# Kernel optimization log

Measured on AMD Instinct MI355X. Metric: run time of the kernel, lower is better.

The kernel has to match this reference:

```python
import jax, jax.numpy as jnp
import numpy as np

N = 50000      # nodes
E = 400000     # edges (before self-loops)
IN = 256       # in_dim
H = 4          # heads in layer 1
C = 64         # h_dim (per-head channels, layer 1)
OUT = 16       # out_dim (layer 2, 1 head)
NEG_SLOPE = 0.2


def gatv2_layer(x, src, dst, Wl, bl, Wr, br, att, bias, heads, ch, concat, num_nodes):
    # x: [N, F]; src/dst: [E']; Wl/Wr: [F, heads*ch]; att: [heads, ch]
    xl = (x @ Wl + bl).reshape(num_nodes, heads, ch)  # source transform
    xr = (x @ Wr + br).reshape(num_nodes, heads, ch)  # target transform
    m = xl[src] + xr[dst]                              # [E', H, C] gather
    e = jnp.sum(jax.nn.leaky_relu(m, NEG_SLOPE) * att, axis=-1)  # [E', H]
    # segment softmax over incoming edges of each dst node (self-loops ensure non-empty)
    emax = jax.ops.segment_max(e, dst, num_segments=num_nodes)   # [N, H]
    ee = jnp.exp(e - emax[dst])
    denom = jax.ops.segment_sum(ee, dst, num_segments=num_nodes)  # [N, H]
    alpha = ee / (denom[dst] + 1e-16)                              # [E', H]
    out = jax.ops.segment_sum(alpha[..., None] * xl[src], dst, num_segments=num_nodes)  # [N,H,C]
    if concat:
        out = out.reshape(num_nodes, heads * ch)
    else:
        out = out.mean(axis=1)
    return out + bias


def setup_inputs() -> dict:
    key = jax.random.key(0)
    ks = jax.random.split(key, 16)
    s = 0.05
    inp = {
        "x": jax.random.normal(ks[0], (N, IN), jnp.float32),
        "edge_index": jax.random.randint(ks[1], (2, E), 0, N),
        # layer 1 params (in_dim -> heads*h_dim)
        "Wl1": jax.random.normal(ks[2], (IN, H * C), jnp.float32) * s,
        "bl1": jnp.zeros((H * C,), jnp.float32),
        "Wr1": jax.random.normal(ks[3], (IN, H * C), jnp.float32) * s,
        "br1": jnp.zeros((H * C,), jnp.float32),
        "att1": jax.random.normal(ks[4], (H, C), jnp.float32) * s,
        "bias1": jnp.zeros((H * C,), jnp.float32),
        # layer 2 params (heads*h_dim -> out_dim, 1 head)
        "Wl2": jax.random.normal(ks[5], (H * C, OUT), jnp.float32) * s,
        "bl2": jnp.zeros((OUT,), jnp.float32),
        "Wr2": jax.random.normal(ks[6], (H * C, OUT), jnp.float32) * s,
        "br2": jnp.zeros((OUT,), jnp.float32),
        "att2": jax.random.normal(ks[7], (1, OUT), jnp.float32) * s,
        "bias2": jnp.zeros((OUT,), jnp.float32),
    }
    return inp


def reference(x, edge_index, Wl1, bl1, Wr1, br1, att1, bias1, Wl2, bl2, Wr2, br2, att2, bias2):
    # add self loops (PyG GATv2Conv default add_self_loops=True)
    loop = jnp.arange(N, dtype=edge_index.dtype)
    src = jnp.concatenate([edge_index[0], loop])
    dst = jnp.concatenate([edge_index[1], loop])
    h = gatv2_layer(x, src, dst, Wl1, bl1, Wr1, br1, att1, bias1, H, C, True, N)
    h = jnp.tanh(h)
    o = gatv2_layer(h, src, dst, Wl2, bl2, Wr2, br2, att2, bias2, 1, OUT, False, N)
    return o, jax.nn.log_softmax(o, axis=1)
```

## Files before the change

kernel.cpp:

```cpp
#include <hip/hip_runtime.h>

typedef __bf16 bfv8 __attribute__((ext_vector_type(8)));
typedef float f32x4 __attribute__((ext_vector_type(4)));
typedef short shortv8 __attribute__((ext_vector_type(8)));

__device__ __forceinline__ float b2f(unsigned short u) {
  unsigned int v = ((unsigned int)u) << 16;
  float f;
  __builtin_memcpy(&f, &v, 4);
  return f;
}
__device__ __forceinline__ unsigned short f2b(float f) {
  unsigned int u;
  __builtin_memcpy(&u, &f, 4);
  u += 0x7fffu + ((u >> 16) & 1u);
  return (unsigned short)(u >> 16);
}

__global__ void probe_kernel(const unsigned short* __restrict__ x, int* __restrict__ flag) {
  int lane = threadIdx.x;
  int cnt = 0;
  for (int i = lane; i < 4096; i += 64) {
    unsigned int e = (x[i] >> 7) & 0xffu;
    if (e >= 0x86u) cnt++;
  }
#pragma unroll
  for (int off = 1; off < 64; off <<= 1) cnt += __shfl_xor(cnt, off, 64);
  if (lane == 0) *flag = (cnt > 100) ? 1 : 0;
}

#define P_TOT 140352
__global__ __launch_bounds__(256) void conv_params_kernel(
    const void* p0, const void* p1, const void* p2, const void* p3,
    const void* p4, const void* p5, const void* p6, const void* p7,
    const void* p8, const void* p9, const void* p10, const void* p11,
    unsigned short* __restrict__ dst, const int* __restrict__ flagp) {
  int i = blockIdx.x * 256 + threadIdx.x;
  if (i >= P_TOT) return;
  const int offs[13] = {0, 65536, 65792, 131328, 131584, 131840, 132096,
                        136192, 136208, 140304, 140320, 140336, P_TOT};
  const void* ptrs[12] = {p0, p1, p2, p3, p4, p5, p6, p7, p8, p9, p10, p11};
  int flag = *flagp;
  int t = 0;
  while (i >= offs[t + 1]) t++;
  int local = i - offs[t];
  unsigned short v;
  if (flag) v = f2b(((const float*)ptrs[t])[local]);
  else v = ((const unsigned short*)ptrs[t])[local];
  dst[i] = v;
}

__global__ __launch_bounds__(256) void transpose_w_kernel(
    const unsigned short* __restrict__ Pc,
    unsigned short* __restrict__ WT1, unsigned short* __restrict__ WT2) {
  int idx = blockIdx.x * 256 + threadIdx.x;
  if (idx < 512 * 256) {
    int n = idx >> 8, k = idx & 255;
    WT1[idx] = (n < 256) ? Pc[0 + k * 256 + n]
                         : Pc[65792 + k * 256 + (n - 256)];
  } else {
    int j = idx - 512 * 256;
    if (j < 32 * 256) {
      int n = j >> 8, k = j & 255;
      WT2[j] = (n < 16) ? Pc[132096 + k * 16 + n]
                        : Pc[136208 + k * 16 + (n - 16)];
    }
  }
}

__global__ __launch_bounds__(256) void gemm1_kernel(
    const void* __restrict__ X, const int* __restrict__ flagp,
    const unsigned short* __restrict__ WT,
    const unsigned short* __restrict__ bl, const unsigned short* __restrict__ br,
    unsigned short* __restrict__ C, int M) {
  __shared__ unsigned short ltile[4][64 * 72];
  const int lane = threadIdx.x & 63;
  const int w = threadIdx.x >> 6;
  const int quad = lane >> 4;
  const int l16 = lane & 15;
  const int m_base = blockIdx.x * 128 + (w >> 1) * 64;
  const int n_base = blockIdx.y * 128 + (w & 1) * 64;
  const int fl = *flagp;

  f32x4 acc[4][4];
#pragma unroll
  for (int i = 0; i < 4; i++)
#pragma unroll
    for (int j = 0; j < 4; j++) acc[i][j] = (f32x4){0.f, 0.f, 0.f, 0.f};

  if (fl) {
    const float* Xf = (const float*)X;
#pragma unroll
    for (int k0 = 0; k0 < 256; k0 += 32) {
      bfv8 a[4], b[4];
#pragma unroll
      for (int i = 0; i < 4; i++) {
        int row = m_base + 16 * i + l16;
        if (row >= M) row = M - 1;
        const float* p = Xf + (size_t)row * 256 + k0 + quad * 8;
        float4 f0 = *reinterpret_cast<const float4*>(p);
        float4 f1 = *reinterpret_cast<const float4*>(p + 4);
        union { bfv8 v; unsigned short us[8]; } pa;
        pa.us[0] = f2b(f0.x); pa.us[1] = f2b(f0.y);
        pa.us[2] = f2b(f0.z); pa.us[3] = f2b(f0.w);
        pa.us[4] = f2b(f1.x); pa.us[5] = f2b(f1.y);
        pa.us[6] = f2b(f1.z); pa.us[7] = f2b(f1.w);
        a[i] = pa.v;
      }
#pragma unroll
      for (int j = 0; j < 4; j++) {
        int col = n_base + 16 * j + l16;
        b[j] = *reinterpret_cast<const bfv8*>(WT + (size_t)col * 256 + k0 + quad * 8);
      }
#pragma unroll
      for (int i = 0; i < 4; i++)
#pragma unroll
        for (int j = 0; j < 4; j++)
          acc[i][j] = __builtin_amdgcn_mfma_f32_16x16x32_bf16(a[i], b[j], acc[i][j], 0, 0, 0);
    }
  } else {
    const unsigned short* Xb = (const unsigned short*)X;
#pragma unroll
    for (int k0 = 0; k0 < 256; k0 += 32) {
      bfv8 a[4], b[4];
#pragma unroll
      for (int i = 0; i < 4; i++) {
        int row = m_base + 16 * i + l16;
        if (row >= M) row = M - 1;
        a[i] = *reinterpret_cast<const bfv8*>(Xb + (size_t)row * 256 + k0 + quad * 8);
      }
#pragma unroll
      for (int j = 0; j < 4; j++) {
        int col = n_base + 16 * j + l16;
        b[j] = *reinterpret_cast<const bfv8*>(WT + (size_t)col * 256 + k0 + quad * 8);
      }
#pragma unroll
      for (int i = 0; i < 4; i++)
#pragma unroll
        for (int j = 0; j < 4; j++)
          acc[i][j] = __builtin_amdgcn_mfma_f32_16x16x32_bf16(a[i], b[j], acc[i][j], 0, 0, 0);
    }
  }

  unsigned short* lt = ltile[w];
#pragma unroll
  for (int j = 0; j < 4; j++) {
    int col = n_base + 16 * j + l16;
    float bias = (col < 256) ? b2f(bl[col]) : b2f(br[col - 256]);
#pragma unroll
    for (int i = 0; i < 4; i++)
#pragma unroll
      for (int r = 0; r < 4; r++)
        lt[(16 * i + quad * 4 + r) * 72 + 16 * j + l16] = f2b(acc[i][j][r] + bias);
  }
#pragma unroll
  for (int pass = 0; pass < 8; pass++) {
    int row = pass * 8 + (lane >> 3);
    int colg = (lane & 7) * 8;
    shortv8 v = *reinterpret_cast<const shortv8*>(lt + row * 72 + colg);
    int grow = m_base + row;
    if (grow < M)
      *reinterpret_cast<shortv8*>(C + (size_t)grow * 512 + n_base + colg) = v;
  }
}

__global__ __launch_bounds__(256) void gemm2_kernel(
    const unsigned short* __restrict__ H, const unsigned short* __restrict__ WT,
    const unsigned short* __restrict__ bl, const unsigned short* __restrict__ br,
    float* __restrict__ C, int M) {
  const int lane = threadIdx.x & 63;
  const int w = threadIdx.x >> 6;
  const int quad = lane >> 4;
  const int l16 = lane & 15;
  const int m_base = blockIdx.x * 256 + w * 64;

  f32x4 acc[4][2];
#pragma unroll
  for (int i = 0; i < 4; i++)
#pragma unroll
    for (int j = 0; j < 2; j++) acc[i][j] = (f32x4){0.f, 0.f, 0.f, 0.f};

#pragma unroll
  for (int k0 = 0; k0 < 256; k0 += 32) {
    bfv8 a[4], b[2];
#pragma unroll
    for (int i = 0; i < 4; i++) {
      int row = m_base + 16 * i + l16;
      if (row >= M) row = M - 1;
      a[i] = *reinterpret_cast<const bfv8*>(H + (size_t)row * 256 + k0 + quad * 8);
    }
#pragma unroll
    for (int j = 0; j < 2; j++) {
      int col = 16 * j + l16;
      b[j] = *reinterpret_cast<const bfv8*>(WT + (size_t)col * 256 + k0 + quad * 8);
    }
#pragma unroll
    for (int i = 0; i < 4; i++)
#pragma unroll
      for (int j = 0; j < 2; j++)
        acc[i][j] = __builtin_amdgcn_mfma_f32_16x16x32_bf16(a[i], b[j], acc[i][j], 0, 0, 0);
  }

#pragma unroll
  for (int j = 0; j < 2; j++) {
    int col = 16 * j + l16;
    float bias = (j == 0) ? b2f(bl[l16]) : b2f(br[l16]);
#pragma unroll
    for (int i = 0; i < 4; i++) {
#pragma unroll
      for (int r = 0; r < 4; r++) {
        int row = m_base + 16 * i + quad * 4 + r;
        if (row < M) C[(size_t)row * 32 + col] = acc[i][j][r] + bias;
      }
    }
  }
}

__global__ __launch_bounds__(256) void count_kernel(const int* __restrict__ ei, int E, int Nn,
                                                    int* __restrict__ cnt) {
  int i = blockIdx.x * 256 + threadIdx.x;
  int total = E + Nn;
  if (i >= total) return;
  int d = (i < E) ? ei[E + i] : (i - E);
  if ((unsigned)d >= (unsigned)Nn) d = 0;
  atomicAdd(&cnt[d], 1);
}

__global__ __launch_bounds__(1024) void scan1_kernel(const int* __restrict__ cnt,
                                                     int* __restrict__ row_start,
                                                     int* __restrict__ blkTot, int Nn) {
  __shared__ int buf[1024];
  int t = threadIdx.x;
  int i = blockIdx.x * 1024 + t;
  int v = (i < Nn) ? cnt[i] : 0;
  buf[t] = v;
  __syncthreads();
  for (int off = 1; off < 1024; off <<= 1) {
    int x = (t >= off) ? buf[t - off] : 0;
    __syncthreads();
    buf[t] += x;
    __syncthreads();
  }
  if (i < Nn) row_start[i] = buf[t] - v;
  if (t == 1023) blkTot[blockIdx.x] = buf[1023];
}

__global__ __launch_bounds__(64) void scan2_kernel(const int* __restrict__ blkTot,
                                                   int* __restrict__ blkOff, int nb,
                                                   int* __restrict__ row_start, int Nn,
                                                   int total) {
  int lane = threadIdx.x;
  int v = (lane < nb) ? blkTot[lane] : 0;
  int s = v;
#pragma unroll
  for (int off = 1; off < 64; off <<= 1) {
    int u = __shfl_up(s, off, 64);
    if (lane >= off) s += u;
  }
  if (lane < nb) blkOff[lane] = s - v;
  if (lane == 0) row_start[Nn] = total;
}

__global__ __launch_bounds__(1024) void scan3_kernel(int* __restrict__ row_start,
                                                     int* __restrict__ cursor,
                                                     const int* __restrict__ blkOff, int Nn) {
  int i = blockIdx.x * 1024 + threadIdx.x;
  if (i < Nn) {
    int val = row_start[i] + blkOff[blockIdx.x];
    row_start[i] = val;
    cursor[i] = val;
  }
}

__global__ __launch_bounds__(256) void fill_kernel(const int* __restrict__ ei, int E, int Nn,
                                                   int* __restrict__ cursor,
                                                   int* __restrict__ csr_src) {
  int i = blockIdx.x * 256 + threadIdx.x;
  int total = E + Nn;
  if (i >= total) return;
  int s, d;
  if (i < E) { s = ei[i]; d = ei[E + i]; } else { s = i - E; d = i - E; }
  if ((unsigned)d >= (unsigned)Nn) d = 0;
  if ((unsigned)s >= (unsigned)Nn) s = 0;
  int pos = atomicAdd(&cursor[d], 1);
  if ((unsigned)pos < (unsigned)total) csr_src[pos] = s;
}

__global__ __launch_bounds__(256) void agg1_kernel(
    const unsigned short* __restrict__ C1,
    const unsigned short* __restrict__ att1,
    const unsigned short* __restrict__ bias1,
    const int* __restrict__ row_start, const int* __restrict__ csr_src,
    unsigned short* __restrict__ H1,
    int Nn, int Etot) {
  int wid = blockIdx.x * 4 + (threadIdx.x >> 6);
  if (wid >= Nn) return;
  int lane = threadIdx.x & 63;
  int c0 = lane * 4;

  ushort4 a4 = *reinterpret_cast<const ushort4*>(att1 + c0);
  float at0 = b2f(a4.x), at1 = b2f(a4.y), at2 = b2f(a4.z), at3 = b2f(a4.w);
  ushort4 r4 = *reinterpret_cast<const ushort4*>(C1 + (size_t)wid * 512 + 256 + c0);
  float xr0 = b2f(r4.x), xr1 = b2f(r4.y), xr2 = b2f(r4.z), xr3 = b2f(r4.w);

  float denom = 0.f, a0 = 0.f, a1 = 0.f, a2 = 0.f, a3 = 0.f;
  int beg = row_start[wid], end = row_start[wid + 1];
  if (beg < 0) beg = 0;
  if (end < beg || end - beg > Etot) end = beg;
  int n = end - beg;

  ushort4 cur0 = make_ushort4(0, 0, 0, 0), cur1 = cur0;
  if (n > 0) {
    int s = csr_src[beg];
    if ((unsigned)s >= (unsigned)Nn) s = 0;
    cur0 = *reinterpret_cast<const ushort4*>(C1 + (size_t)s * 512 + c0);
  }
  if (n > 1) {
    int s = csr_src[beg + 1];
    if ((unsigned)s >= (unsigned)Nn) s = 0;
    cur1 = *reinterpret_cast<const ushort4*>(C1 + (size_t)s * 512 + c0);
  }

#define AGG1_BODY(XV)                                                        \
  {                                                                          \
    float xl0 = b2f(XV.x), xl1 = b2f(XV.y), xl2 = b2f(XV.z), xl3 = b2f(XV.w); \
    float m0 = xl0 + xr0, m1 = xl1 + xr1, m2 = xl2 + xr2, m3 = xl3 + xr3;    \
    float l0 = m0 > 0.f ? m0 : 0.2f * m0;                                    \
    float l1 = m1 > 0.f ? m1 : 0.2f * m1;                                    \
    float l2 = m2 > 0.f ? m2 : 0.2f * m2;                                    \
    float l3 = m3 > 0.f ? m3 : 0.2f * m3;                                    \
    float part = l0 * at0 + l1 * at1 + l2 * at2 + l3 * at3;                  \
    part += __shfl_xor(part, 1, 64);                                         \
    part += __shfl_xor(part, 2, 64);                                         \
    part += __shfl_xor(part, 4, 64);                                         \
    part += __shfl_xor(part, 8, 64);                                         \
    part = fminf(fmaxf(part, -60.f), 60.f);                                  \
    float wgt = __expf(part);                                                \
    denom += wgt;                                                            \
    a0 += wgt * xl0; a1 += wgt * xl1; a2 += wgt * xl2; a3 += wgt * xl3;      \
  }

  int i = 0;
  for (; i + 2 <= n; i += 2) {
    ushort4 nxt0 = cur0, nxt1 = cur1;
    int q0 = beg + i + 2, q1 = beg + i + 3;
    if (q0 < end) {
      int s = csr_src[q0];
      if ((unsigned)s >= (unsigned)Nn) s = 0;
      nxt0 = *reinterpret_cast<const ushort4*>(C1 + (size_t)s * 512 + c0);
    }
    if (q1 < end) {
      int s = csr_src[q1];
      if ((unsigned)s >= (unsigned)Nn) s = 0;
      nxt1 = *reinterpret_cast<const ushort4*>(C1 + (size_t)s * 512 + c0);
    }
    AGG1_BODY(cur0);
    AGG1_BODY(cur1);
    cur0 = nxt0;
    cur1 = nxt1;
  }
  if (i < n) AGG1_BODY(cur0);
#undef AGG1_BODY

  float inv = 1.f / (denom + 1e-16f);
  ushort4 b4 = *reinterpret_cast<const ushort4*>(bias1 + c0);
  float h0 = tanhf(a0 * inv + b2f(b4.x));
  float h1 = tanhf(a1 * inv + b2f(b4.y));
  float h2 = tanhf(a2 * inv + b2f(b4.z));
  float h3 = tanhf(a3 * inv + b2f(b4.w));
  if (!(h0 == h0)) h0 = 0.f;
  if (!(h1 == h1)) h1 = 0.f;
  if (!(h2 == h2)) h2 = 0.f;
  if (!(h3 == h3)) h3 = 0.f;
  ushort4 o4;
  o4.x = f2b(h0); o4.y = f2b(h1); o4.z = f2b(h2); o4.w = f2b(h3);
  *reinterpret_cast<ushort4*>(H1 + (size_t)wid * 256 + c0) = o4;
}

__global__ __launch_bounds__(256) void agg2_kernel(
    const float* __restrict__ C2,
    const unsigned short* __restrict__ att2,
    const unsigned short* __restrict__ bias2,
    const int* __restrict__ row_start, const int* __restrict__ csr_src,
    float* __restrict__ out,
    int Nn, int Etot) {
  int wid = blockIdx.x * 4 + (threadIdx.x >> 6);
  if (wid >= Nn) return;
  int lane = threadIdx.x & 63;
  int g = lane >> 4;
  int c = lane & 15;

  float att = b2f(att2[c]);
  float xr = C2[(size_t)wid * 32 + 16 + c];
  float denom = 0.f, acc = 0.f;
  int beg = row_start[wid], end = row_start[wid + 1];
  if (beg < 0) beg = 0;
  if (end < beg || end - beg > Etot) end = beg;

  int p = beg + g;
  float xl_cur = 0.f;
  if (p < end) {
    int s = csr_src[p];
    if ((unsigned)s >= (unsigned)Nn) s = 0;
    xl_cur = C2[(size_t)s * 32 + c];
  }
  while (p < end) {
    int pn = p + 4;
    float xl_nxt = 0.f;
    if (pn < end) {
      int s = csr_src[pn];
      if ((unsigned)s >= (unsigned)Nn) s = 0;
      xl_nxt = C2[(size_t)s * 32 + c];
    }
    float mm = xl_cur + xr;
    float lr = mm > 0.f ? mm : 0.2f * mm;
    float part = lr * att;
    part += __shfl_xor(part, 1, 64);
    part += __shfl_xor(part, 2, 64);
    part += __shfl_xor(part, 4, 64);
    part += __shfl_xor(part, 8, 64);
    part = fminf(fmaxf(part, -60.f), 60.f);
    float wgt = __expf(part);
    denom += wgt;
    acc += wgt * xl_cur;
    xl_cur = xl_nxt;
    p = pn;
  }
  denom += __shfl_xor(denom, 16, 64);
  denom += __shfl_xor(denom, 32, 64);
  acc += __shfl_xor(acc, 16, 64);
  acc += __shfl_xor(acc, 32, 64);

  float o = acc / (denom + 1e-16f) + b2f(bias2[c]);
  if (!(o == o)) o = 0.f;
  float mx = o;
  mx = fmaxf(mx, __shfl_xor(mx, 1, 64));
  mx = fmaxf(mx, __shfl_xor(mx, 2, 64));
  mx = fmaxf(mx, __shfl_xor(mx, 4, 64));
  mx = fmaxf(mx, __shfl_xor(mx, 8, 64));
  float ex = expf(o - mx);
  float se = ex;
  se += __shfl_xor(se, 1, 64);
  se += __shfl_xor(se, 2, 64);
  se += __shfl_xor(se, 4, 64);
  se += __shfl_xor(se, 8, 64);
  float ls = logf(se);
  if (lane < 16) {
    out[(size_t)wid * 16 + c] = o;
    out[(size_t)Nn * 16 + (size_t)wid * 16 + c] = o - mx - ls;
  }
}

extern "C" void kernel_launch(void* const* d_in, const int* in_sizes, int n_in,
                              void* d_out, int out_size, void* d_ws, size_t ws_size,
                              hipStream_t stream) {
  const void* x_raw = d_in[0];
  const int* ei     = (const int*)d_in[1];

  const int M = in_sizes[0] / 256;
  const int E = in_sizes[1] / 2;
  const int TOT = E + M;

  char* ws = (char*)d_ws;
  size_t off = 0;
  auto alloc = [&](size_t bytes) -> void* {
    void* p = ws + off;
    off = (off + bytes + 255) & ~(size_t)255;
    return p;
  };
  int*            flag   = (int*)alloc(4);
  unsigned short* Pc     = (unsigned short*)alloc((size_t)P_TOT * 2);
  unsigned short* WT1    = (unsigned short*)alloc((size_t)512 * 256 * 2);
  unsigned short* WT2    = (unsigned short*)alloc((size_t)32 * 256 * 2);
  int*            cnt    = (int*)alloc((size_t)M * 4);
  int*            cursor = (int*)alloc((size_t)M * 4);
  int*            row_start = (int*)alloc((size_t)(M + 1) * 4);
  int*            csr_src   = (int*)alloc((size_t)TOT * 4);
  int*            blkTot = (int*)alloc(64 * 4);
  int*            blkOff = (int*)alloc(64 * 4);
  float*          C2     = (float*)alloc((size_t)M * 32 * 4);
  unsigned short* C1     = (unsigned short*)alloc((size_t)M * 512 * 2);
  unsigned short* H1     = (unsigned short*)alloc((size_t)M * 256 * 2);
  const size_t need = off;
  (void)n_in;

  if (ws_size < need) {
    hipMemsetAsync(d_out, 0, (size_t)out_size * 4, stream);
    return;
  }

  unsigned short* bl1c   = Pc + 65536;
  unsigned short* br1c   = Pc + 131328;
  unsigned short* att1c  = Pc + 131584;
  unsigned short* bias1c = Pc + 131840;
  unsigned short* bl2c   = Pc + 136192;
  unsigned short* br2c   = Pc + 140304;
  unsigned short* att2c  = Pc + 140320;
  unsigned short* bias2c = Pc + 140336;

  hipMemsetAsync(cnt, 0, (size_t)M * 4, stream);

  probe_kernel<<<1, 64, 0, stream>>>((const unsigned short*)x_raw, flag);
  conv_params_kernel<<<(P_TOT + 255) / 256, 256, 0, stream>>>(
      d_in[2], d_in[3], d_in[4], d_in[5], d_in[6], d_in[7], d_in[8], d_in[9],
      d_in[10], d_in[11], d_in[12], d_in[13], Pc, flag);

  transpose_w_kernel<<<(512 * 256 + 32 * 256 + 255) / 256, 256, 0, stream>>>(Pc, WT1, WT2);

  dim3 g1((M + 127) / 128, 4);
  gemm1_kernel<<<g1, 256, 0, stream>>>(x_raw, flag, WT1, bl1c, br1c, C1, M);

  count_kernel<<<(TOT + 255) / 256, 256, 0, stream>>>(ei, E, M, cnt);
  int nb = (M + 1023) / 1024;
  scan1_kernel<<<nb, 1024, 0, stream>>>(cnt, row_start, blkTot, M);
  scan2_kernel<<<1, 64, 0, stream>>>(blkTot, blkOff, nb, row_start, M, TOT);
  scan3_kernel<<<nb, 1024, 0, stream>>>(row_start, cursor, blkOff, M);
  fill_kernel<<<(TOT + 255) / 256, 256, 0, stream>>>(ei, E, M, cursor, csr_src);

  agg1_kernel<<<(M + 3) / 4, 256, 0, stream>>>(C1, att1c, bias1c, row_start, csr_src,
                                               H1, M, TOT);

  gemm2_kernel<<<(M + 255) / 256, 256, 0, stream>>>(H1, WT2, bl2c, br2c, C2, M);

  agg2_kernel<<<(M + 3) / 4, 256, 0, stream>>>(C2, att2c, bias2c, row_start, csr_src,
                                               (float*)d_out, M, TOT);
}
```

Measured before the change: 343.6 us.

## Pre-convert X to bf16, stage weight tiles in swizzled LDS, reorder GEMM1 grid

Adds a separate kernel that converts the fp32 input X to bf16 once, so GEMM1 no longer converts it inline four times (once per N-block). GEMM1 now loads its 128-column weight tile through double-buffered, XOR-swizzled shared memory instead of reading it directly from global memory. The grid is transposed so blocks sharing the same rows of X run adjacently, which should improve cache reuse of X. The cost is an extra pass over X in memory and additional barriers in GEMM1. The H1 buffer now reuses the Xc workspace.

```diff
diff --git a/kernel.cpp b/kernel.cpp
--- a/kernel.cpp
+++ b/kernel.cpp
@@ -27,6 +27,22 @@
 #pragma unroll
   for (int off = 1; off < 64; off <<= 1) cnt += __shfl_xor(cnt, off, 64);
   if (lane == 0) *flag = (cnt > 100) ? 1 : 0;
+}
+
+__global__ __launch_bounds__(256) void conv_x_kernel(const void* __restrict__ x,
+                                                     unsigned short* __restrict__ dst,
+                                                     const int* __restrict__ flagp, int n) {
+  int i = (blockIdx.x * 256 + threadIdx.x) * 4;
+  if (i >= n) return;
+  if (*flagp) {
+    float4 f = *reinterpret_cast<const float4*>((const float*)x + i);
+    ushort4 o;
+    o.x = f2b(f.x); o.y = f2b(f.y); o.z = f2b(f.z); o.w = f2b(f.w);
+    *reinterpret_cast<ushort4*>(dst + i) = o;
+  } else {
+    *reinterpret_cast<ushort4*>(dst + i) =
+        *reinterpret_cast<const ushort4*>((const unsigned short*)x + i);
+  }
 }
 
 #define P_TOT 140352
@@ -69,18 +85,24 @@
 }
 
 __global__ __launch_bounds__(256) void gemm1_kernel(
-    const void* __restrict__ X, const int* __restrict__ flagp,
+    const unsigned short* __restrict__ X,
     const unsigned short* __restrict__ WT,
     const unsigned short* __restrict__ bl, const unsigned short* __restrict__ br,
     unsigned short* __restrict__ C, int M) {
-  __shared__ unsigned short ltile[4][64 * 72];
-  const int lane = threadIdx.x & 63;
-  const int w = threadIdx.x >> 6;
+  __shared__ unsigned short smem[18432];
+  const int t = threadIdx.x;
+  const int lane = t & 63;
+  const int w = t >> 6;
   const int quad = lane >> 4;
   const int l16 = lane & 15;
-  const int m_base = blockIdx.x * 128 + (w >> 1) * 64;
-  const int n_base = blockIdx.y * 128 + (w & 1) * 64;
-  const int fl = *flagp;
+  const int n_blk = blockIdx.x;
+  const int m_base = blockIdx.y * 128 + (w >> 1) * 64;
+  const int n_base = n_blk * 128 + (w & 1) * 64;
+
+  const int st_row = t >> 3;
+  const int st_seg = t & 7;
+  const unsigned short* wt_base =
+      WT + ((size_t)(n_blk * 128 + st_row)) * 256 + st_seg * 8;
 
   f32x4 acc[4][4];
 #pragma unroll
@@ -88,29 +110,41 @@
 #pragma unroll
     for (int j = 0; j < 4; j++) acc[i][j] = (f32x4){0.f, 0.f, 0.f, 0.f};
 
-  if (fl) {
-    const float* Xf = (const float*)X;
-#pragma unroll
-    for (int k0 = 0; k0 < 256; k0 += 32) {
+  shortv8 st[4];
+#pragma unroll
+  for (int i = 0; i < 4; i++)
+    st[i] = *reinterpret_cast<const shortv8*>(wt_base + (size_t)(32 * i) * 256);
+#pragma unroll
+  for (int i = 0; i < 4; i++) {
+    int row = st_row + 32 * i;
+    *reinterpret_cast<shortv8*>(smem + row * 64 + ((st_seg ^ (row & 7)) * 8)) = st[i];
+  }
+  __syncthreads();
+
+#pragma unroll
+  for (int c = 0; c < 4; c++) {
+    if (c < 3) {
+#pragma unroll
+      for (int i = 0; i < 4; i++)
+        st[i] = *reinterpret_cast<const shortv8*>(wt_base + (size_t)(32 * i) * 256 +
+                                                  (c + 1) * 64);
+    }
+    const unsigned short* bb = smem + (c & 1) * 8192;
+#pragma unroll
+    for (int sub = 0; sub < 2; sub++) {
       bfv8 a[4], b[4];
+      int seg_r = sub * 4 + quad;
 #pragma unroll
       for (int i = 0; i < 4; i++) {
         int row = m_base + 16 * i + l16;
         if (row >= M) row = M - 1;
-        const float* p = Xf + (size_t)row * 256 + k0 + quad * 8;
-        float4 f0 = *reinterpret_cast<const float4*>(p);
-        float4 f1 = *reinterpret_cast<const float4*>(p + 4);
-        union { bfv8 v; unsigned short us[8]; } pa;
-        pa.us[0] = f2b(f0.x); pa.us[1] = f2b(f0.y);
-        pa.us[2] = f2b(f0.z); pa.us[3] = f2b(f0.w);
-        pa.us[4] = f2b(f1.x); pa.us[5] = f2b(f1.y);
-        pa.us[6] = f2b(f1.z); pa.us[7] = f2b(f1.w);
-        a[i] = pa.v;
+        a[i] = *reinterpret_cast<const bfv8*>(X + (size_t)row * 256 + c * 64 + sub * 32 +
+                                              quad * 8);
       }
 #pragma unroll
       for (int j = 0; j < 4; j++) {
-        int col = n_base + 16 * j + l16;
-        b[j] = *reinterpret_cast<const bfv8*>(WT + (size_t)col * 256 + k0 + quad * 8);
+        int col = (w & 1) * 64 + 16 * j + l16;
+        b[j] = *reinterpret_cast<const bfv8*>(bb + col * 64 + ((seg_r ^ (col & 7)) * 8));
       }
 #pragma unroll
       for (int i = 0; i < 4; i++)
@@ -118,31 +152,20 @@
         for (int j = 0; j < 4; j++)
           acc[i][j] = __builtin_amdgcn_mfma_f32_16x16x32_bf16(a[i], b[j], acc[i][j], 0, 0, 0);
     }
-  } else {
-    const unsigned short* Xb = (const unsigned short*)X;
-#pragma unroll
-    for (int k0 = 0; k0 < 256; k0 += 32) {
-      bfv8 a[4], b[4];
+    if (c < 3) {
+      int buf = (c + 1) & 1;
 #pragma unroll
       for (int i = 0; i < 4; i++) {
-        int row = m_base + 16 * i + l16;
-        if (row >= M) row = M - 1;
-        a[i] = *reinterpret_cast<const bfv8*>(Xb + (size_t)row * 256 + k0 + quad * 8);
+        int row = st_row + 32 * i;
+        *reinterpret_cast<shortv8*>(smem + buf * 8192 + row * 64 +
+                                    ((st_seg ^ (row & 7)) * 8)) = st[i];
       }
-#pragma unroll
-      for (int j = 0; j < 4; j++) {
-        int col = n_base + 16 * j + l16;
-        b[j] = *reinterpret_cast<const bfv8*>(WT + (size_t)col * 256 + k0 + quad * 8);
-      }
-#pragma unroll
-      for (int i = 0; i < 4; i++)
-#pragma unroll
-        for (int j = 0; j < 4; j++)
-          acc[i][j] = __builtin_amdgcn_mfma_f32_16x16x32_bf16(a[i], b[j], acc[i][j], 0, 0, 0);
-    }
-  }
-
-  unsigned short* lt = ltile[w];
+      __syncthreads();
+    }
+  }
+
+  __syncthreads();
+  unsigned short* lt = smem + w * 4608;
 #pragma unroll
   for (int j = 0; j < 4; j++) {
     int col = n_base + 16 * j + l16;
@@ -160,7 +183,8 @@
     shortv8 v = *reinterpret_cast<const shortv8*>(lt + row * 72 + colg);
     int grow = m_base + row;
     if (grow < M)
-      *reinterpret_cast<shortv8*>(C + (size_t)grow * 512 + n_base + colg) = v;
+      *reinterpret_cast<shortv8*>(C + (size_t)grow * 512 + n_base - (w & 1) * 64 +
+                                  (w & 1) * 64 + colg) = v;
   }
 }
 
@@ -460,6 +484,7 @@
   const int M = in_sizes[0] / 256;
   const int E = in_sizes[1] / 2;
   const int TOT = E + M;
+  const int NX = M * 256;
 
   char* ws = (char*)d_ws;
   size_t off = 0;
@@ -470,6 +495,7 @@
   };
   int*            flag   = (int*)alloc(4);
   unsigned short* Pc     = (unsigned short*)alloc((size_t)P_TOT * 2);
+  unsigned short* Xc     = (unsigned short*)alloc((size_t)NX * 2);
   unsigned short* WT1    = (unsigned short*)alloc((size_t)512 * 256 * 2);
   unsigned short* WT2    = (unsigned short*)alloc((size_t)32 * 256 * 2);
   int*            cnt    = (int*)alloc((size_t)M * 4);
@@ -480,9 +506,9 @@
   int*            blkOff = (int*)alloc(64 * 4);
   float*          C2     = (float*)alloc((size_t)M * 32 * 4);
   unsigned short* C1     = (unsigned short*)alloc((size_t)M * 512 * 2);
-  unsigned short* H1     = (unsigned short*)alloc((size_t)M * 256 * 2);
   const size_t need = off;
   (void)n_in;
+  unsigned short* H1 = Xc;
 
   if (ws_size < need) {
     hipMemsetAsync(d_out, 0, (size_t)out_size * 4, stream);
@@ -501,14 +527,15 @@
   hipMemsetAsync(cnt, 0, (size_t)M * 4, stream);
 
   probe_kernel<<<1, 64, 0, stream>>>((const unsigned short*)x_raw, flag);
+  conv_x_kernel<<<(NX / 4 + 255) / 256, 256, 0, stream>>>(x_raw, Xc, flag, NX);
   conv_params_kernel<<<(P_TOT + 255) / 256, 256, 0, stream>>>(
       d_in[2], d_in[3], d_in[4], d_in[5], d_in[6], d_in[7], d_in[8], d_in[9],
       d_in[10], d_in[11], d_in[12], d_in[13], Pc, flag);
 
   transpose_w_kernel<<<(512 * 256 + 32 * 256 + 255) / 256, 256, 0, stream>>>(Pc, WT1, WT2);
 
-  dim3 g1((M + 127) / 128, 4);
-  gemm1_kernel<<<g1, 256, 0, stream>>>(x_raw, flag, WT1, bl1c, br1c, C1, M);
+  dim3 g1(4, (M + 127) / 128);
+  gemm1_kernel<<<g1, 256, 0, stream>>>(Xc, WT1, bl1c, br1c, C1, M);
 
   count_kernel<<<(TOT + 255) / 256, 256, 0, stream>>>(ei, E, M, cnt);
   int nb = (M + 1023) / 1024;
```

After: 316.0 us. -8.0%, faster.
